# Performance work log

Measured on AMD Instinct MI355X. Metric: run time of the kernel, lower is better.

The kernel has to match this reference:

```python
import jax, jax.numpy as jnp
import numpy as np

B, T, D, U = 64, 512, 1024, 128


def setup_inputs() -> dict:
    key = jax.random.key(0)
    k1, k2, k3, k4, k5 = jax.random.split(key, 5)
    x = jax.random.normal(k1, (B, T, D), dtype=jnp.float32)
    mask = jnp.ones((B, T), dtype=jnp.int32)
    # learned parameters (glorot-ish scale for kernel)
    kernel = jax.random.normal(k2, (D, U), dtype=jnp.float32) * (1.0 / np.sqrt(D))
    bias = jnp.zeros((U,), dtype=jnp.float32)
    left_boundary = jax.random.normal(k3, (U,), dtype=jnp.float32) * 0.1
    right_boundary = jax.random.normal(k4, (U,), dtype=jnp.float32) * 0.1
    return {"x": x, "mask": mask, "kernel": kernel, "bias": bias,
            "left_boundary": left_boundary, "right_boundary": right_boundary}


def _shift_right(m):  # [B,T,1] -> pad one zero step at front along time
    return jnp.concatenate([jnp.zeros_like(m[:, :1]), m[:, :-1]], axis=1)


def _shift_left(m):  # [B,T,1] -> pad one zero step at end along time
    return jnp.concatenate([m[:, 1:], jnp.zeros_like(m[:, :1])], axis=1)


def reference(x, mask, kernel, bias, left_boundary, right_boundary):
    # input energy: linear activation of dense projection  [B,T,U]
    energy = jnp.einsum('btd,du->btu', x, kernel) + bias
    # boundary energies with mask (faithful to source semantics)
    m = mask.astype(energy.dtype)[:, :, None]                     # [B,T,1]
    start_mask = (m > _shift_right(m)).astype(energy.dtype)       # first valid step
    end_mask = (_shift_left(m) > m).astype(energy.dtype)          # as written in source
    energy = energy + start_mask * left_boundary[None, None, :]
    energy = energy + end_mask * right_boundary[None, None, :]
    return energy
```

## Files before the change

kernel.cpp:

```cpp
#include <hip/hip_runtime.h>

#define TT 512
#define DD 1024
#define UU 128
#define MM 32768

typedef short short8 __attribute__((ext_vector_type(8)));
typedef float f32x4 __attribute__((ext_vector_type(4)));

__device__ __forceinline__ unsigned short f2bf(float f) {
    union { float f; unsigned u; } v; v.f = f;
    unsigned u = v.u;
    return (unsigned short)((u + 0x7fffu + ((u >> 16) & 1u)) >> 16);
}

__global__ __launch_bounds__(256) void wprep_kernel(const float* __restrict__ w,
                                                    unsigned short* __restrict__ wt) {
    int tg = blockIdx.x * 256 + threadIdx.x;
    int kg = tg & 7;
    int n  = (tg >> 3) & 127;
    int kc = tg >> 10;
    union { unsigned short s[8]; uint4 v; } o;
#pragma unroll
    for (int j = 0; j < 8; ++j) {
        int k = kc * 64 + kg * 8 + j;
        o.s[j] = f2bf(w[k * 128 + n]);
    }
    *(uint4*)(wt + tg * 8) = o.v;
}

__global__ __launch_bounds__(256, 4) void crf_energy_kernel(
    const float* __restrict__ x,
    const int* __restrict__ mask,
    const unsigned short* __restrict__ wt,
    const float* __restrict__ bias,
    const float* __restrict__ lb,
    const float* __restrict__ rb,
    float* __restrict__ out)
{
    const int tid  = threadIdx.x;
    const int wave = tid >> 6;
    const int lane = tid & 63;
    const int q    = lane >> 4;
    const int r    = lane & 15;

    const int mt   = wave >> 1;
    const int nh   = wave & 1;
    const int row0 = blockIdx.x * 32 + mt * 16;

    const float* __restrict__ xrow = x + (size_t)(row0 + r) * DD;
    const unsigned short* __restrict__ wbase = wt + (size_t)(nh * 64 + r) * 64 + q * 8;

    f32x4 acc[4];
#pragma unroll
    for (int nt = 0; nt < 4; ++nt) acc[nt] = (f32x4){0.f, 0.f, 0.f, 0.f};

    float4 araw[2][2];
#pragma unroll
    for (int ks = 0; ks < 2; ++ks) {
        const float* p = xrow + ks * 32 + q * 8;
        araw[ks][0] = *(const float4*)(p);
        araw[ks][1] = *(const float4*)(p + 4);
    }

#pragma unroll 2
    for (int kc = 0; kc < 16; ++kc) {
        const int kcn = (kc < 15) ? kc + 1 : kc;
        float4 anxt[2][2];
#pragma unroll
        for (int ks = 0; ks < 2; ++ks) {
            const float* p = xrow + kcn * 64 + ks * 32 + q * 8;
            anxt[ks][0] = *(const float4*)(p);
            anxt[ks][1] = *(const float4*)(p + 4);
        }

        short8 afrag[2];
#pragma unroll
        for (int ks = 0; ks < 2; ++ks) {
            union { unsigned short s[8]; short8 v; } pk;
            pk.s[0] = f2bf(araw[ks][0].x); pk.s[1] = f2bf(araw[ks][0].y);
            pk.s[2] = f2bf(araw[ks][0].z); pk.s[3] = f2bf(araw[ks][0].w);
            pk.s[4] = f2bf(araw[ks][1].x); pk.s[5] = f2bf(araw[ks][1].y);
            pk.s[6] = f2bf(araw[ks][1].z); pk.s[7] = f2bf(araw[ks][1].w);
            afrag[ks] = pk.v;
        }

        const unsigned short* wkc = wbase + (size_t)kc * 8192;
#pragma unroll
        for (int ks = 0; ks < 2; ++ks) {
            short8 b[4];
#pragma unroll
            for (int nt = 0; nt < 4; ++nt)
                b[nt] = *(const short8*)(wkc + nt * 1024 + ks * 32);
#pragma unroll
            for (int nt = 0; nt < 4; ++nt)
                acc[nt] = __builtin_amdgcn_mfma_f32_16x16x32_bf16(
                    afrag[ks], b[nt], acc[nt], 0, 0, 0);
        }

#pragma unroll
        for (int ks = 0; ks < 2; ++ks) {
            araw[ks][0] = anxt[ks][0];
            araw[ks][1] = anxt[ks][1];
        }
    }

#pragma unroll
    for (int nt = 0; nt < 4; ++nt) {
        const int n = nh * 64 + nt * 16 + r;
        const float bi  = bias[n];
        const float lbn = lb[n];
        const float rbn = rb[n];
#pragma unroll
        for (int reg = 0; reg < 4; ++reg) {
            const int m = row0 + q * 4 + reg;
            const int t = m & (TT - 1);
            const int cur  = mask[m];
            const int prev = (t != 0)      ? mask[m - 1] : 0;
            const int nxt  = (t != TT - 1) ? mask[m + 1] : 0;
            float e = acc[nt][reg] + bi;
            if (cur > prev) e += lbn;
            if (nxt > cur)  e += rbn;
            out[(size_t)m * UU + n] = e;
        }
    }
}

extern "C" void kernel_launch(void* const* d_in, const int* in_sizes, int n_in,
                              void* d_out, int out_size, void* d_ws, size_t ws_size,
                              hipStream_t stream) {
    const float* x    = (const float*)d_in[0];
    const int*   mask = (const int*)d_in[1];
    const float* w    = (const float*)d_in[2];
    const float* bias = (const float*)d_in[3];
    const float* lb   = (const float*)d_in[4];
    const float* rb   = (const float*)d_in[5];
    float* out = (float*)d_out;
    unsigned short* wt = (unsigned short*)d_ws;

    wprep_kernel<<<64, 256, 0, stream>>>(w, wt);
    crf_energy_kernel<<<1024, 256, 0, stream>>>(x, mask, wt, bias, lb, rb, out);
}
```

Before: 254.4 us.

## Stage A and B tiles through LDS with register prefetch double buffering

```diff
diff --git a/kernel.cpp b/kernel.cpp
--- a/kernel.cpp
+++ b/kernel.cpp
@@ -4,6 +4,10 @@
 #define DD 1024
 #define UU 128
 #define MM 32768
+#define BK 64
+#define NCHUNK 16
+#define LDA 68
+#define LDB 68
 
 typedef short short8 __attribute__((ext_vector_type(8)));
 typedef float f32x4 __attribute__((ext_vector_type(4)));
@@ -38,6 +42,9 @@
     const float* __restrict__ rb,
     float* __restrict__ out)
 {
+    __shared__ unsigned short lA[32 * LDA];
+    __shared__ unsigned short lB[128 * LDB];
+
     const int tid  = threadIdx.x;
     const int wave = tid >> 6;
     const int lane = tid & 63;
@@ -46,81 +53,79 @@
 
     const int mt   = wave >> 1;
     const int nh   = wave & 1;
-    const int row0 = blockIdx.x * 32 + mt * 16;
+    const int row0 = blockIdx.x * 32;
 
-    const float* __restrict__ xrow = x + (size_t)(row0 + r) * DD;
-    const unsigned short* __restrict__ wbase = wt + (size_t)(nh * 64 + r) * 64 + q * 8;
+    const int ma = tid >> 3, ka = tid & 7;
+    const float* __restrict__ xsrc = x + (size_t)(row0 + ma) * DD + ka * 8;
+    const int nb = tid >> 1, hb = tid & 1;
+    const unsigned short* __restrict__ wsrc = wt + nb * 64 + hb * 32;
+    unsigned short* const lAdst = &lA[ma * LDA + ka * 8];
+    unsigned short* const lBdst = &lB[nb * LDB + hb * 32];
 
     f32x4 acc[4];
 #pragma unroll
     for (int nt = 0; nt < 4; ++nt) acc[nt] = (f32x4){0.f, 0.f, 0.f, 0.f};
 
-    float4 araw[2][2];
+    float4 apf[2][2];
+    uint4  bpf[2][4];
+
+    apf[0][0] = *(const float4*)(xsrc);
+    apf[0][1] = *(const float4*)(xsrc + 4);
 #pragma unroll
-    for (int ks = 0; ks < 2; ++ks) {
-        const float* p = xrow + ks * 32 + q * 8;
-        araw[ks][0] = *(const float4*)(p);
-        araw[ks][1] = *(const float4*)(p + 4);
-    }
+    for (int u = 0; u < 4; ++u) bpf[0][u] = *(const uint4*)(wsrc + u * 8);
 
-#pragma unroll 2
-    for (int kc = 0; kc < 16; ++kc) {
-        const int kcn = (kc < 15) ? kc + 1 : kc;
-        float4 anxt[2][2];
 #pragma unroll
-        for (int ks = 0; ks < 2; ++ks) {
-            const float* p = xrow + kcn * 64 + ks * 32 + q * 8;
-            anxt[ks][0] = *(const float4*)(p);
-            anxt[ks][1] = *(const float4*)(p + 4);
+    for (int kc = 0; kc < NCHUNK; ++kc) {
+        const int cur = kc & 1, nxt = cur ^ 1;
+
+        {
+            union { unsigned short s[8]; uint4 v; } pk;
+            pk.s[0] = f2bf(apf[cur][0].x); pk.s[1] = f2bf(apf[cur][0].y);
+            pk.s[2] = f2bf(apf[cur][0].z); pk.s[3] = f2bf(apf[cur][0].w);
+            pk.s[4] = f2bf(apf[cur][1].x); pk.s[5] = f2bf(apf[cur][1].y);
+            pk.s[6] = f2bf(apf[cur][1].z); pk.s[7] = f2bf(apf[cur][1].w);
+            *(uint4*)lAdst = pk.v;
         }
+#pragma unroll
+        for (int u = 0; u < 4; ++u) *(uint4*)(lBdst + u * 8) = bpf[cur][u];
+        __syncthreads();
 
-        short8 afrag[2];
+        if (kc < NCHUNK - 1) {
+            const float* xs = xsrc + (kc + 1) * BK;
+            apf[nxt][0] = *(const float4*)(xs);
+            apf[nxt][1] = *(const float4*)(xs + 4);
+            const unsigned short* ws = wsrc + (size_t)(kc + 1) * 8192;
 #pragma unroll
-        for (int ks = 0; ks < 2; ++ks) {
-            union { unsigned short s[8]; short8 v; } pk;
-            pk.s[0] = f2bf(araw[ks][0].x); pk.s[1] = f2bf(araw[ks][0].y);
-            pk.s[2] = f2bf(araw[ks][0].z); pk.s[3] = f2bf(araw[ks][0].w);
-            pk.s[4] = f2bf(araw[ks][1].x); pk.s[5] = f2bf(araw[ks][1].y);
-            pk.s[6] = f2bf(araw[ks][1].z); pk.s[7] = f2bf(araw[ks][1].w);
-            afrag[ks] = pk.v;
-        }
-
-        const unsigned short* wkc = wbase + (size_t)kc * 8192;
-#pragma unroll
-        for (int ks = 0; ks < 2; ++ks) {
-            short8 b[4];
-#pragma unroll
-            for (int nt = 0; nt < 4; ++nt)
-                b[nt] = *(const short8*)(wkc + nt * 1024 + ks * 32);
-#pragma unroll
-            for (int nt = 0; nt < 4; ++nt)
-                acc[nt] = __builtin_amdgcn_mfma_f32_16x16x32_bf16(
-                    afrag[ks], b[nt], acc[nt], 0, 0, 0);
+            for (int u = 0; u < 4; ++u) bpf[nxt][u] = *(const uint4*)(ws + u * 8);
         }
 
 #pragma unroll
         for (int ks = 0; ks < 2; ++ks) {
-            araw[ks][0] = anxt[ks][0];
-            araw[ks][1] = anxt[ks][1];
+            short8 a = *(const short8*)(&lA[(mt * 16 + r) * LDA + ks * 32 + q * 8]);
+            short8 b[4];
+#pragma unroll
+            for (int nt = 0; nt < 4; ++nt)
+                b[nt] = *(const short8*)(&lB[(nh * 64 + nt * 16 + r) * LDB + ks * 32 + q * 8]);
+#pragma unroll
+            for (int nt = 0; nt < 4; ++nt)
+                acc[nt] = __builtin_amdgcn_mfma_f32_16x16x32_bf16(a, b[nt], acc[nt], 0, 0, 0);
         }
+        __syncthreads();
     }
 
 #pragma unroll
-    for (int nt = 0; nt < 4; ++nt) {
-        const int n = nh * 64 + nt * 16 + r;
-        const float bi  = bias[n];
-        const float lbn = lb[n];
-        const float rbn = rb[n];
+    for (int reg = 0; reg < 4; ++reg) {
+        const int m = row0 + mt * 16 + q * 4 + reg;
+        const int t = m & (TT - 1);
+        const int cur  = mask[m];
+        const int prev = (t != 0)      ? mask[m - 1] : 0;
+        const int nxt  = (t != TT - 1) ? mask[m + 1] : 0;
+        const float sm = (cur > prev) ? 1.f : 0.f;
+        const float em = (nxt > cur)  ? 1.f : 0.f;
 #pragma unroll
-        for (int reg = 0; reg < 4; ++reg) {
-            const int m = row0 + q * 4 + reg;
-            const int t = m & (TT - 1);
-            const int cur  = mask[m];
-            const int prev = (t != 0)      ? mask[m - 1] : 0;
-            const int nxt  = (t != TT - 1) ? mask[m + 1] : 0;
-            float e = acc[nt][reg] + bi;
-            if (cur > prev) e += lbn;
-            if (nxt > cur)  e += rbn;
+        for (int nt = 0; nt < 4; ++nt) {
+            const int n = nh * 64 + nt * 16 + r;
+            float e = acc[nt][reg] + bias[n] + sm * lb[n] + em * rb[n];
             out[(size_t)m * UU + n] = e;
         }
     }
```

Measured after the change: 283.5 us. 11.4% more time.
